# Optimization experiments

Hardware: AMD Instinct MI355X
Metric: run time of the kernel (lower is better)

## Reference

```python
import jax, jax.numpy as jnp
import numpy as np

NP_, NB_, E_, BE_ = 10000, 30000, 300000, 8192
PIN, BIN, EA = 128, 128, 16
HID, GH = 64, 4
D, TH, L, NC, SEQ = 128, 4, 2, 10, 6


def _ln(x, g, b, eps=1e-5):
    m = x.mean(-1, keepdims=True)
    v = ((x - m) ** 2).mean(-1, keepdims=True)
    return (x - m) * jax.lax.rsqrt(v + eps) * g + b


def _seg_softmax(e, seg, n):
    m = jax.ops.segment_max(e, seg, num_segments=n)
    m = jnp.where(jnp.isfinite(m), m, 0.0)
    ex = jnp.exp(e - m[seg])
    s = jax.ops.segment_sum(ex, seg, num_segments=n)
    return ex / (s[seg] + 1e-16)


def _gatv2(xs, xd, es, ed, ea, Wl, bl, Wr, br, We, att, bias, n_dst):
    # PyG GATv2Conv, concat=False, add_self_loops=False, eval mode (no dropout)
    xl = (xs @ Wl + bl).reshape(-1, GH, HID)   # [Ns,H,C] source transform (message content)
    xr = (xd @ Wr + br).reshape(-1, GH, HID)   # [Nd,H,C] dest transform
    eh = (ea @ We).reshape(-1, GH, HID)        # [E,H,C] edge transform (no bias in PyG)
    msg = xl[es] + xr[ed] + eh                 # [E,H,C]
    score = jnp.einsum('ehc,hc->eh', jax.nn.leaky_relu(msg, 0.2), att)
    alpha = _seg_softmax(score, ed, n_dst)     # softmax over in-edges per dest node
    out = jax.ops.segment_sum(alpha[..., None] * xl[es], ed, num_segments=n_dst)
    return out.mean(axis=1) + bias             # concat=False -> mean over heads


def _mha(x, Wqkv, bqkv, Wo, bo):
    S, d = x.shape
    dh = d // TH
    q, k, v = jnp.split(x @ Wqkv + bqkv, 3, axis=-1)
    q = q.reshape(S, TH, dh).transpose(1, 0, 2)
    k = k.reshape(S, TH, dh).transpose(1, 0, 2)
    v = v.reshape(S, TH, dh).transpose(1, 0, 2)
    a = jax.nn.softmax(jnp.einsum('hqd,hkd->hqk', q, k) / jnp.sqrt(jnp.float32(dh)), axis=-1)
    o = jnp.einsum('hqk,hkd->hqd', a, v).transpose(1, 0, 2).reshape(S, d)
    return o @ Wo + bo


def _forward(pitcher_feat, batter_feat, edge_attr, history_states,
             Wp, bp, Wb, bb,
             rel_Wl, rel_bl, rel_Wr, rel_br, rel_We, rel_att, rel_bias,
             rev_Wl, rev_bl, rev_Wr, rev_br, rev_We, rev_att, rev_bias,
             Wgs, bgs, Wet, bet, pos,
             Wqkv, bqkv, Wo, bo, ln1g, ln1b, W1, b1, W2, b2, ln2g, ln2b,
             Wc1, bc1, Wc2, bc2,
             edge_src, edge_dst, edge_ids):
    gelu = lambda t: jax.nn.gelu(t, approximate=False)
    px = gelu(pitcher_feat @ Wp + bp)
    bx = gelu(batter_feat @ Wb + bb)
    # ('pitcher','faces','batter'): messages pitcher->batter, aggregated at batter nodes
    h_b = gelu(_gatv2(px, bx, edge_src, edge_dst, edge_attr,
                      rel_Wl, rel_bl, rel_Wr, rel_br, rel_We, rel_att, rel_bias, bx.shape[0]))
    # reversed relation: batter->pitcher, aggregated at pitcher nodes
    h_p = gelu(_gatv2(bx, px, edge_dst, edge_src, edge_attr,
                      rev_Wl, rev_bl, rev_Wr, rev_br, rev_We, rev_att, rev_bias, px.shape[0]))
    state = jnp.concatenate([h_p.mean(0), h_b.mean(0), edge_attr.mean(0)], -1) @ Wgs + bgs
    tok = jnp.concatenate([h_p[edge_src[edge_ids]], h_b[edge_dst[edge_ids]],
                           edge_attr[edge_ids]], -1) @ Wet + bet
    x = jnp.concatenate([history_states, state[None]], 0) + pos[:SEQ]
    for i in range(L):  # post-LN TransformerEncoderLayer, gelu activation, eval (no dropout)
        x = _ln(x + _mha(x, Wqkv[i], bqkv[i], Wo[i], bo[i]), ln1g[i], ln1b[i])
        f = gelu(x @ W1[i] + b1[i]) @ W2[i] + b2[i]
        x = _ln(x + f, ln2g[i], ln2b[i])
    ctx = x[-1]
    cat = jnp.concatenate([tok, jnp.broadcast_to(ctx, (tok.shape[0], D))], -1)
    return gelu(cat @ Wc1 + bc1) @ Wc2 + bc2


def setup_inputs() -> dict:
    key = jax.random.key(0)
    ks = iter(jax.random.split(key, 64))
    nrm = lambda shape, s: jax.random.normal(next(ks), shape, dtype=jnp.float32) * s
    d = {
        'pitcher_feat': nrm((NP_, PIN), 1.0),
        'batter_feat': nrm((NB_, BIN), 1.0),
        'edge_attr': nrm((E_, EA), 1.0),
        'history_states': nrm((SEQ - 1, D), 1.0),
        'Wp': nrm((PIN, HID), 0.05), 'bp': jnp.zeros((HID,), jnp.float32),
        'Wb': nrm((BIN, HID), 0.05), 'bb': jnp.zeros((HID,), jnp.float32),
    }
    for p in ('rel', 'rev'):
        d[p + '_Wl'] = nrm((HID, GH * HID), 0.05)
        d[p + '_bl'] = jnp.zeros((GH * HID,), jnp.float32)
        d[p + '_Wr'] = nrm((HID, GH * HID), 0.05)
        d[p + '_br'] = jnp.zeros((GH * HID,), jnp.float32)
        d[p + '_We'] = nrm((EA, GH * HID), 0.05)
        d[p + '_att'] = nrm((GH, HID), 0.05)
        d[p + '_bias'] = jnp.zeros((HID,), jnp.float32)
    cin = 2 * HID + EA
    d['Wgs'] = nrm((cin, D), 0.05); d['bgs'] = jnp.zeros((D,), jnp.float32)
    d['Wet'] = nrm((cin, D), 0.05); d['bet'] = jnp.zeros((D,), jnp.float32)
    d['pos'] = nrm((SEQ, D), 0.02)
    d['Wqkv'] = nrm((L, D, 3 * D), 0.05); d['bqkv'] = jnp.zeros((L, 3 * D), jnp.float32)
    d['Wo'] = nrm((L, D, D), 0.05); d['bo'] = jnp.zeros((L, D), jnp.float32)
    d['ln1g'] = jnp.ones((L, D), jnp.float32); d['ln1b'] = jnp.zeros((L, D), jnp.float32)
    d['W1'] = nrm((L, D, 4 * D), 0.05); d['b1'] = jnp.zeros((L, 4 * D), jnp.float32)
    d['W2'] = nrm((L, 4 * D, D), 0.05); d['b2'] = jnp.zeros((L, D), jnp.float32)
    d['ln2g'] = jnp.ones((L, D), jnp.float32); d['ln2b'] = jnp.zeros((L, D), jnp.float32)
    d['Wc1'] = nrm((2 * D, D), 0.05); d['bc1'] = jnp.zeros((D,), jnp.float32)
    d['Wc2'] = nrm((D, NC), 0.05); d['bc2'] = jnp.zeros((NC,), jnp.float32)
    d['edge_src'] = jax.random.randint(next(ks), (E_,), 0, NP_)
    d['edge_dst'] = jax.random.randint(next(ks), (E_,), 0, NB_)
    d['edge_ids'] = jax.random.randint(next(ks), (BE_,), 0, E_)
    return d


def reference(pitcher_feat, batter_feat, edge_attr, history_states,
              Wp, bp, Wb, bb,
              rel_Wl, rel_bl, rel_Wr, rel_br, rel_We, rel_att, rel_bias,
              rev_Wl, rev_bl, rev_Wr, rev_br, rev_We, rev_att, rev_bias,
              Wgs, bgs, Wet, bet, pos,
              Wqkv, bqkv, Wo, bo, ln1g, ln1b, W1, b1, W2, b2, ln2g, ln2b,
              Wc1, bc1, Wc2, bc2,
              edge_src, edge_dst, edge_ids):
    return _forward(pitcher_feat, batter_feat, edge_attr, history_states,
                    Wp, bp, Wb, bb,
                    rel_Wl, rel_bl, rel_Wr, rel_br, rel_We, rel_att, rel_bias,
                    rev_Wl, rev_bl, rev_Wr, rev_br, rev_We, rev_att, rev_bias,
                    Wgs, bgs, Wet, bet, pos,
                    Wqkv, bqkv, Wo, bo, ln1g, ln1b, W1, b1, W2, b2, ln2g, ln2b,
                    Wc1, bc1, Wc2, bc2,
                    edge_src, edge_dst, edge_ids)
```

## Files before the change

### kernel.cpp

```cpp
#include <hip/hip_runtime.h>
#include <math.h>

#define NP 10000
#define NB 30000
#define NEDGE 300000
#define BEDGE 8192
#define EAD 16
#define HID 64
#define GH 4
#define CW 256
#define DD 128
#define SEQ 6
#define NCLS 10
#define L 2
#define NEACOL 64

#if defined(__has_builtin)
#  if __has_builtin(__builtin_amdgcn_fdot2)
#    define HAVE_DOT2 1
#  else
#    define HAVE_DOT2 0
#  endif
#else
#  define HAVE_DOT2 0
// ... 355 lines not shown
    sWeH[i] = __builtin_bit_cast(int,
        __builtin_amdgcn_cvt_pkrtz(We[(2*j)*CW + c], We[(2*j+1)*CW + c]));
  }
#else
  for (int i = t*4; i < 16*CW; i += 1024)
    *(float4*)&sWeH[i] = *(const float4*)&We[i];
#endif
  __syncthreads();
  float4 at = *(const float4*)&att[4*l];
  float4 bi = *(const float4*)&bias[(l & 15)*4];
  float cs0 = 0.f, cs1 = 0.f, cs2 = 0.f, cs3 = 0.f;
  int wid = bid*4 + (t >> 6);
  int nw = nblk*4;
  for (int d = wid; d < ndst; d += nw){
    ushort4 ru = *(const ushort4*)(xr + (size_t)d*CW + 4*l);
    float r0 = b2f(ru.x), r1 = b2f(ru.y), r2 = b2f(ru.z), r3 = b2f(ru.w);
    int rs = row_start[d], re = row_start[d+1];
    float s = 0.f;
    float a0 = 0.f, a1 = 0.f, a2 = 0.f, a3 = 0.f;
    if (rs < re){
      int last = re - 1;
      #define CLMP(x) ((x) > last ? last : (x))
      int2 qA0 = csr[rs],         qA1 = csr[CLMP(rs+1)];
      int2 qB0 = csr[CLMP(rs+2)], qB1 = csr[CLMP(rs+3)];
      int2 nA0 = csr[CLMP(rs+4)], nA1 = csr[CLMP(rs+5)];
      int2 nB0 = csr[CLMP(rs+6)], nB1 = csr[CLMP(rs+7)];
      ushort4 xA0 = *(const ushort4*)(xl + (size_t)qA0.y*CW + 4*l);
      ushort4 xA1 = *(const ushort4*)(xl + (size_t)qA1.y*CW + 4*l);
      evt_t  evA0 = evload(ea, qA0.x, l);
      evt_t  evA1 = evload(ea, qA1.x, l);
      ushort4 xB0 = *(const ushort4*)(xl + (size_t)qB0.y*CW + 4*l);
      ushort4 xB1 = *(const ushort4*)(xl + (size_t)qB1.y*CW + 4*l);
      evt_t  evB0 = evload(ea, qB0.x, l);
      evt_t  evB1 = evload(ea, qB1.x, l);
      for (int i = rs; i < re; i += 4){
        int2 mA0 = csr[CLMP(i+8)],  mA1 = csr[CLMP(i+9)];
        int2 mB0 = csr[CLMP(i+10)], mB1 = csr[CLMP(i+11)];
        GAT_PAIR(xA0, xA1, evA0, evA1, (i+1 < re), true);
        xA0 = *(const ushort4*)(xl + (size_t)nA0.y*CW + 4*l);
        xA1 = *(const ushort4*)(xl + (size_t)nA1.y*CW + 4*l);
        evA0 = evload(ea, nA0.x, l);
        evA1 = evload(ea, nA1.x, l);
        nA0 = mA0; nA1 = mA1;
        GAT_PAIR(xB0, xB1, evB0, evB1, (i+3 < re), (i+2 < re));
        xB0 = *(const ushort4*)(xl + (size_t)nB0.y*CW + 4*l);
        xB1 = *(const ushort4*)(xl + (size_t)nB1.y*CW + 4*l);
        evB0 = evload(ea, nB0.x, l);
        evB1 = evload(ea, nB1.x, l);
        nB0 = mB0; nB1 = mB1;
      }
      #undef CLMP
    }
    float inv = 1.f / (s + 1e-16f);
    float v0 = a0*inv, v1 = a1*inv, v2 = a2*inv, v3 = a3*inv;
    v0 += __shfl_xor(v0, 16); v1 += __shfl_xor(v1, 16);
    v2 += __shfl_xor(v2, 16); v3 += __shfl_xor(v3, 16);
    v0 += __shfl_xor(v0, 32); v1 += __shfl_xor(v1, 32);
    v2 += __shfl_xor(v2, 32); v3 += __shfl_xor(v3, 32);
    if (l < 16){
      float4 o;
      o.x = geluf(v0*0.25f + bi.x);
      o.y = geluf(v1*0.25f + bi.y);
      o.z = geluf(v2*0.25f + bi.z);
      o.w = geluf(v3*0.25f + bi.w);
      *(float4*)(hout + (size_t)d*HID + 4*l) = o;
      cs0 += o.x; cs1 += o.y; cs2 += o.z; cs3 += o.w;
    }
  }
  int w = t >> 6;
  if (l < 16){
    csum[w][l][0] = cs0; csum[w][l][1] = cs1;
    csum[w][l][2] = cs2; csum[w][l][3] = cs3;
  }
  __syncthreads();
  if (t < 64){
    int lq = t >> 2, j = t & 3;
    float sum = csum[0][lq][j] + csum[1][lq][j] + csum[2][lq][j] + csum[3][lq][j];
    float scale = isA ? (1.f/NB) : (1.f/NP);
    float* dst = isA ? (mvec + 64) : mvec;
    atomicAdd(&dst[t], sum * scale);
  }
}

__device__ void gemmcat_body(int bid, const float* __restrict__ hp, const float* __restrict__ hb,
                             const float* __restrict__ ea, const int* __restrict__ esrc,
                             const int* __restrict__ edst, const int* __restrict__ eids,
                             const float* __restrict__ W, const float* __restrict__ bias,
                             float* __restrict__ out)
{
  __shared__ float sAT[16][68];
  __shared__ float sB[16][68];
  __shared__ int sS[64], sD[64], sE[64];
  int t = threadIdx.x;
  int m0 = (bid >> 1)*64, n0 = (bid & 1)*64;
  if (t < 64){
    int e = eids[m0 + t];
    sS[t] = esrc[e]; sD[t] = edst[e]; sE[t] = e;
  }
  __syncthreads();
  int tr = t >> 4, tc = t & 15;
  float acc[4][4] = {};
  for (int k0 = 0; k0 < 144; k0 += 16){
    {
      int r = t >> 2, c = (t & 3) * 4;
      const float* src; int col = k0 + c;
      if (k0 < 64)       { src = hp + (size_t)sS[r]*HID; }
      else if (k0 < 128) { src = hb + (size_t)sD[r]*HID; col -= 64; }
      else               { src = ea + (size_t)sE[r]*EAD; col -= 128; }
      float4 va = *(const float4*)(src + col);
      sAT[c+0][r] = va.x; sAT[c+1][r] = va.y; sAT[c+2][r] = va.z; sAT[c+3][r] = va.w;
    }
    {
      int r = t >> 4, c = (t & 15) * 4;
      float4 vb = *(const float4*)(W + (size_t)(k0+r)*DD + n0 + c);
      *(float4*)&sB[r][c] = vb;
    }
    __syncthreads();
    #pragma unroll
    for (int k = 0; k < 16; ++k){
      float4 av = *(const float4*)&sAT[k][tr*4];
      float4 bv = *(const float4*)&sB[k][tc*4];
      acc[0][0] = fmaf(av.x, bv.x, acc[0][0]);
      acc[0][1] = fmaf(av.x, bv.y, acc[0][1]);
      acc[0][2] = fmaf(av.x, bv.z, acc[0][2]);
      acc[0][3] = fmaf(av.x, bv.w, acc[0][3]);
      acc[1][0] = fmaf(av.y, bv.x, acc[1][0]);
      acc[1][1] = fmaf(av.y, bv.y, acc[1][1]);
      acc[1][2] = fmaf(av.y, bv.z, acc[1][2]);
      acc[1][3] = fmaf(av.y, bv.w, acc[1][3]);
      acc[2][0] = fmaf(av.z, bv.x, acc[2][0]);
      acc[2][1] = fmaf(av.z, bv.y, acc[2][1]);
      acc[2][2] = fmaf(av.z, bv.z, acc[2][2]);
      acc[2][3] = fmaf(av.z, bv.w, acc[2][3]);
      acc[3][0] = fmaf(av.w, bv.x, acc[3][0]);
      acc[3][1] = fmaf(av.w, bv.y, acc[3][1]);
      acc[3][2] = fmaf(av.w, bv.z, acc[3][2]);
      acc[3][3] = fmaf(av.w, bv.w, acc[3][3]);
    }
    __syncthreads();
  }
  #pragma unroll
  for (int i = 0; i < 4; ++i){
    int gr = m0 + tr*4 + i;
    float4 v;
    v.x = acc[i][0] + bias[n0 + tc*4 + 0];
    v.y = acc[i][1] + bias[n0 + tc*4 + 1];
    v.z = acc[i][2] + bias[n0 + tc*4 + 2];
    v.w = acc[i][3] + bias[n0 + tc*4 + 3];
    *(float4*)(out + (size_t)gr*DD + n0 + tc*4) = v;
  }
}

__global__ __launch_bounds__(256)
void gemmcat_kernel(const float* __restrict__ hp, const float* __restrict__ hb,
                    const float* __restrict__ ea, const int* __restrict__ esrc,
                    const int* __restrict__ edst, const int* __restrict__ eids,
                    const float* __restrict__ Wet, const float* __restrict__ bet,
                    float* __restrict__ tokb)
{
  gemmcat_body(blockIdx.x, hp, hb, ea, esrc, edst, eids, Wet, bet, tokb);
}

template<int K, int N, int NC>
__device__ __forceinline__ void qstageF(const float* __restrict__ x,
                                        const float* __restrict__ W,
                                        float (&a)[6][4], int q, int ch)
{
  constexpr int NQ = N/4;
  constexpr int KC = K/NC;
  constexpr int J  = KC/4;
  const float4* wp = (const float4*)W + (size_t)(ch*KC)*NQ + q;
  const float* xb = x + ch*KC;
  float4 wv[KC];
  int kx[J];
  #pragma unroll
  for (int j = 0; j < J; ++j){
    int k4 = (j + ch) & (J-1);
    kx[j] = k4;
    wv[j*4+0] = wp[(size_t)(k4*4+0)*NQ];
    wv[j*4+1] = wp[(size_t)(k4*4+1)*NQ];
    wv[j*4+2] = wp[(size_t)(k4*4+2)*NQ];
    wv[j*4+3] = wp[(size_t)(k4*4+3)*NQ];
  }
  #pragma unroll
  for (int s = 0; s < 6; ++s){ a[s][0]=0.f; a[s][1]=0.f; a[s][2]=0.f; a[s][3]=0.f; }
  #pragma unroll
  for (int j = 0; j < J; ++j){
    #pragma unroll
    for (int s = 0; s < 6; ++s){
      float4 xv = *(const float4*)&xb[s*K + kx[j]*4];
      a[s][0]=fmaf(xv.x,wv[j*4+0].x,a[s][0]); a[s][0]=fmaf(xv.y,wv[j*4+1].x,a[s][0]);
      a[s][0]=fmaf(xv.z,wv[j*4+2].x,a[s][0]); a[s][0]=fmaf(xv.w,wv[j*4+3].x,a[s][0]);
      a[s][1]=fmaf(xv.x,wv[j*4+0].y,a[s][1]); a[s][1]=fmaf(xv.y,wv[j*4+1].y,a[s][1]);
      a[s][1]=fmaf(xv.z,wv[j*4+2].y,a[s][1]); a[s][1]=fmaf(xv.w,wv[j*4+3].y,a[s][1]);
      a[s][2]=fmaf(xv.x,wv[j*4+0].z,a[s][2]); a[s][2]=fmaf(xv.y,wv[j*4+1].z,a[s][2]);
      a[s][2]=fmaf(xv.z,wv[j*4+2].z,a[s][2]); a[s][2]=fmaf(xv.w,wv[j*4+3].z,a[s][2]);
      a[s][3]=fmaf(xv.x,wv[j*4+0].w,a[s][3]); a[s][3]=fmaf(xv.y,wv[j*4+1].w,a[s][3]);
      a[s][3]=fmaf(xv.z,wv[j*4+2].w,a[s][3]); a[s][3]=fmaf(xv.w,wv[j*4+3].w,a[s][3]);
    }
  }
  #pragma unroll
  for (int off = 1; off < NC; off <<= 1){
    #pragma unroll
    for (int s = 0; s < 6; ++s){
      a[s][0]+=__shfl_xor(a[s][0],off); a[s][1]+=__shfl_xor(a[s][1],off);
      a[s][2]+=__shfl_xor(a[s][2],off); a[s][3]+=__shfl_xor(a[s][3],off);
    }
  }
}

__global__ __launch_bounds__(512)
void xform_kernel(const float* __restrict__ hist, const float* __restrict__ mvec,
                  const float* __restrict__ Wgs, const float* __restrict__ bgs,
                  const float* __restrict__ pos,
                  const float* __restrict__ Wqkv, const float* __restrict__ bqkv,
                  const float* __restrict__ Wo, const float* __restrict__ bo,
                  const float* __restrict__ ln1g, const float* __restrict__ ln1b,
                  const float* __restrict__ W1, const float* __restrict__ b1,
                  const float* __restrict__ W2, const float* __restrict__ b2,
                  const float* __restrict__ ln2g, const float* __restrict__ ln2b,
                  const float* __restrict__ Wc1, const float* __restrict__ bc1,
                  float* __restrict__ bias2)
{
  __shared__ float sx[SEQ*DD];
  __shared__ float sq[SEQ*3*DD];
  __shared__ float sh[SEQ*512];
  __shared__ float st[SEQ*DD];
  __shared__ float sc[4][6][6];
  __shared__ float smv[144];
  int t = threadIdx.x;

  for (int i = t; i < (SEQ-1)*DD; i += 512) sx[i] = hist[i] + pos[i];
  if (t < 144) smv[t] = mvec[t];
  __syncthreads();
  if (t < 256){
    int q = t >> 3, ch = t & 7;
    float4 wv[18];
    #pragma unroll
    for (int kk = 0; kk < 18; ++kk)
      wv[kk] = *(const float4*)&Wgs[(ch*18+kk)*DD + q*4];
    float a0=0.f,a1=0.f,a2=0.f,a3=0.f;
    #pragma unroll
    for (int kk = 0; kk < 18; ++kk){
      float xv = smv[ch*18+kk];
      a0=fmaf(xv,wv[kk].x,a0); a1=fmaf(xv,wv[kk].y,a1);
      a2=fmaf(xv,wv[kk].z,a2); a3=fmaf(xv,wv[kk].w,a3);
    }
    #pragma unroll
    for (int off = 1; off < 8; off <<= 1){
      a0+=__shfl_xor(a0,off); a1+=__shfl_xor(a1,off);
      a2+=__shfl_xor(a2,off); a3+=__shfl_xor(a3,off);
    }
    if (ch == 0){
      int n = q*4, base = (SEQ-1)*DD + n;
      sx[base+0]=a0+bgs[n+0]+pos[base+0];
      sx[base+1]=a1+bgs[n+1]+pos[base+1];
      sx[base+2]=a2+bgs[n+2]+pos[base+2];
      sx[base+3]=a3+bgs[n+3]+pos[base+3];
    }
  }
  __syncthreads();

  for (int lyr = 0; lyr < L; ++lyr){
    if (t < 384){
      int q = t >> 2, ch = t & 3;
      const float* wq = Wqkv + (size_t)lyr*DD*3*DD;
      const float* bq = bqkv + lyr*3*DD;
      float a[6][4];
      qstageF<128,384,4>(sx, wq, a, q, ch);
      if (ch == 0){
        int n = q*4;
        #pragma unroll
        for (int s = 0; s < 6; ++s){
          sq[s*384+n+0]=a[s][0]+bq[n+0];
          sq[s*384+n+1]=a[s][1]+bq[n+1];
          sq[s*384+n+2]=a[s][2]+bq[n+2];
          sq[s*384+n+3]=a[s][3]+bq[n+3];
        }
      }
    }
    __syncthreads();
    if (t < 144){
      int h = t/36, r = t%36, qi = r/6, ki = r%6;
      float acc = 0.f;
      #pragma unroll
      for (int d2 = 0; d2 < 32; ++d2)
        acc = fmaf(sq[qi*384 + h*32 + d2], sq[ki*384 + 128 + h*32 + d2], acc);
      sc[h][qi][ki] = acc * 0.17677669529663687f;
    }
    __syncthreads();
    if (t < 24){
      int h = t/6, qi = t%6;
      float* row = sc[h][qi];
      float mx = row[0];
      #pragma unroll
      for (int k = 1; k < 6; ++k) mx = fmaxf(mx, row[k]);
      float sm = 0.f;
      #pragma unroll
      for (int k = 0; k < 6; ++k){ row[k] = __expf(row[k]-mx); sm += row[k]; }
      float inv = 1.f/sm;
      #pragma unroll
      for (int k = 0; k < 6; ++k) row[k] *= inv;
    }
    __syncthreads();
    for (int i = t; i < SEQ*DD; i += 512){
      int s = i >> 7, n = i & 127, h = n >> 5, d2 = n & 31;
      float acc = 0.f;
      #pragma unroll
      for (int ki = 0; ki < 6; ++ki)
        acc = fmaf(sc[h][s][ki], sq[ki*384 + 256 + h*32 + d2], acc);
      st[i] = acc;
    }
    __syncthreads();
    {
      int q = t >> 4, ch = t & 15;
      float a[6][4];
      qstageF<128,128,16>(st, Wo + (size_t)lyr*DD*DD, a, q, ch);
      if (ch == 0){
        int n = q*4;
        const float* bop = bo + lyr*DD;
        #pragma unroll
        for (int s = 0; s < 6; ++s){
          sh[s*128+n+0]=a[s][0]+bop[n+0]+sx[s*128+n+0];
          sh[s*128+n+1]=a[s][1]+bop[n+1]+sx[s*128+n+1];
          sh[s*128+n+2]=a[s][2]+bop[n+2]+sx[s*128+n+2];
          sh[s*128+n+3]=a[s][3]+bop[n+3]+sx[s*128+n+3];
        }
      }
    }
    __syncthreads();
    {
      int w = t >> 6, lw = t & 63;
      if (w < SEQ){
        const float* g = ln1g + lyr*DD; const float* be = ln1b + lyr*DD;
        float v0 = sh[w*DD + lw], v1 = sh[w*DD + 64 + lw];
        float sm = v0 + v1;
        #pragma unroll
        for (int off = 1; off < 64; off <<= 1) sm += __shfl_xor(sm, off);
        float mean = sm * 0.0078125f;
        float d0 = v0-mean, d1 = v1-mean;
        float qv = d0*d0 + d1*d1;
        #pragma unroll
        for (int off = 1; off < 64; off <<= 1) qv += __shfl_xor(qv, off);
        float inv = rsqrtf(qv*0.0078125f + 1e-5f);
        sx[w*DD + lw]      = d0*inv*g[lw] + be[lw];
        sx[w*DD + 64 + lw] = d1*inv*g[64+lw] + be[64+lw];
      }
    }
    __syncthreads();
    {
      int q = t >> 2, ch = t & 3;
      const float* w1 = W1 + (size_t)lyr*DD*512;
      const float* b1p = b1 + lyr*512;
      float a[6][4];
      qstageF<128,512,4>(sx, w1, a, q, ch);
      if (ch == 0){
        int n = q*4;
        #pragma unroll
        for (int s = 0; s < 6; ++s){
          sh[s*512+n+0]=geluf(a[s][0]+b1p[n+0]);
          sh[s*512+n+1]=geluf(a[s][1]+b1p[n+1]);
          sh[s*512+n+2]=geluf(a[s][2]+b1p[n+2]);
          sh[s*512+n+3]=geluf(a[s][3]+b1p[n+3]);
        }
      }
    }
    __syncthreads();
    {
      int q = t >> 4, ch = t & 15;
      const float* w2 = W2 + (size_t)lyr*512*DD;
      const float* b2p = b2 + lyr*DD;
      float a[6][4];
      qstageF<512,128,16>(sh, w2, a, q, ch);
      if (ch == 0){
        int n = q*4;
        #pragma unroll
        for (int s = 0; s < 6; ++s){
          st[s*128+n+0]=a[s][0]+b2p[n+0]+sx[s*128+n+0];
          st[s*128+n+1]=a[s][1]+b2p[n+1]+sx[s*128+n+1];
          st[s*128+n+2]=a[s][2]+b2p[n+2]+sx[s*128+n+2];
          st[s*128+n+3]=a[s][3]+b2p[n+3]+sx[s*128+n+3];
        }
      }
    }
    __syncthreads();
    {
      int w = t >> 6, lw = t & 63;
      if (w < SEQ){
        const float* g = ln2g + lyr*DD; const float* be = ln2b + lyr*DD;
        float v0 = st[w*DD + lw], v1 = st[w*DD + 64 + lw];
        float sm = v0 + v1;
        #pragma unroll
        for (int off = 1; off < 64; off <<= 1) sm += __shfl_xor(sm, off);
        float mean = sm * 0.0078125f;
        float d0 = v0-mean, d1 = v1-mean;
        float qv = d0*d0 + d1*d1;
        #pragma unroll
        for (int off = 1; off < 64; off <<= 1) qv += __shfl_xor(qv, off);
        float inv = rsqrtf(qv*0.0078125f + 1e-5f);
        sx[w*DD + lw]      = d0*inv*g[lw] + be[lw];
        sx[w*DD + 64 + lw] = d1*inv*g[64+lw] + be[64+lw];
      }
    }
    __syncthreads();
  }
  if (t < 256){
    int q = t >> 3, ch = t & 7;
    const float4* wp = (const float4*)(Wc1 + (size_t)DD*DD) + (size_t)(ch*16)*32 + q;
    const float* xb = &sx[(SEQ-1)*DD + ch*16];
    float4 wv[16];
    int kx[4];
    #pragma unroll
    for (int j = 0; j < 4; ++j){
      int k4 = (j + ch) & 3;
      kx[j] = k4;
      wv[j*4+0] = wp[(size_t)(k4*4+0)*32];
      wv[j*4+1] = wp[(size_t)(k4*4+1)*32];
      wv[j*4+2] = wp[(size_t)(k4*4+2)*32];
      wv[j*4+3] = wp[(size_t)(k4*4+3)*32];
    }
    float a0=0.f,a1=0.f,a2=0.f,a3=0.f;
    #pragma unroll
    for (int j = 0; j < 4; ++j){
      float4 xv = *(const float4*)&xb[kx[j]*4];
      a0=fmaf(xv.x,wv[j*4+0].x,a0); a0=fmaf(xv.y,wv[j*4+1].x,a0);
      a0=fmaf(xv.z,wv[j*4+2].x,a0); a0=fmaf(xv.w,wv[j*4+3].x,a0);
      a1=fmaf(xv.x,wv[j*4+0].y,a1); a1=fmaf(xv.y,wv[j*4+1].y,a1);
      a1=fmaf(xv.z,wv[j*4+2].y,a1); a1=fmaf(xv.w,wv[j*4+3].y,a1);
      a2=fmaf(xv.x,wv[j*4+0].z,a2); a2=fmaf(xv.y,wv[j*4+1].z,a2);
      a2=fmaf(xv.z,wv[j*4+2].z,a2); a2=fmaf(xv.w,wv[j*4+3].z,a2);
      a3=fmaf(xv.x,wv[j*4+0].w,a3); a3=fmaf(xv.y,wv[j*4+1].w,a3);
      a3=fmaf(xv.z,wv[j*4+2].w,a3); a3=fmaf(xv.w,wv[j*4+3].w,a3);
    }
    #pragma unroll
    for (int off = 1; off < 8; off <<= 1){
      a0+=__shfl_xor(a0,off); a1+=__shfl_xor(a1,off);
      a2+=__shfl_xor(a2,off); a3+=__shfl_xor(a3,off);
    }
    if (ch == 0){
      int n = q*4;
      bias2[n+0]=a0+bc1[n+0];
      bias2[n+1]=a1+bc1[n+1];
      bias2[n+2]=a2+bc1[n+2];
      bias2[n+3]=a3+bc1[n+3];
    }
  }
}

__global__ __launch_bounds__(256)
void cls_kernel(const float* __restrict__ A, const float* __restrict__ W,
                const float* __restrict__ bias2, const float* __restrict__ Wc2,
                const float* __restrict__ bc2, float* __restrict__ out)
{
  __shared__ float sAT[16][68];
  __shared__ float sB[16][132];
  __shared__ float sH[64][129];
  int t = threadIdx.x;
  int m0 = blockIdx.x * 64;
  int tr = t >> 4, tc = t & 15;
  float acc[4][8] = {};
  for (int k0 = 0; k0 < DD; k0 += 16){
    {
      int r = t >> 2, c = (t & 3) * 4;
      float4 va = *(const float4*)(A + (size_t)(m0+r)*DD + k0 + c);
      sAT[c+0][r] = va.x; sAT[c+1][r] = va.y; sAT[c+2][r] = va.z; sAT[c+3][r] = va.w;
    }
    {
      int r = t >> 4, c = (t & 15) * 8;
      float4 b0 = *(const float4*)(W + (size_t)(k0+r)*DD + c);
      float4 b1 = *(const float4*)(W + (size_t)(k0+r)*DD + c + 4);
      *(float4*)&sB[r][c] = b0;
      *(float4*)&sB[r][c+4] = b1;
    }
    __syncthreads();
    #pragma unroll
    for (int k = 0; k < 16; ++k){
      float4 av = *(const float4*)&sAT[k][tr*4];
      float4 b0 = *(const float4*)&sB[k][tc*8];
      float4 b1 = *(const float4*)&sB[k][tc*8+4];
      #pragma unroll
      for (int i = 0; i < 4; ++i){
        float avi = (i==0)?av.x:(i==1)?av.y:(i==2)?av.z:av.w;
        acc[i][0] = fmaf(avi, b0.x, acc[i][0]);
        acc[i][1] = fmaf(avi, b0.y, acc[i][1]);
        acc[i][2] = fmaf(avi, b0.z, acc[i][2]);
        acc[i][3] = fmaf(avi, b0.w, acc[i][3]);
        acc[i][4] = fmaf(avi, b1.x, acc[i][4]);
        acc[i][5] = fmaf(avi, b1.y, acc[i][5]);
        acc[i][6] = fmaf(avi, b1.z, acc[i][6]);
        acc[i][7] = fmaf(avi, b1.w, acc[i][7]);
      }
    }
    __syncthreads();
  }
  #pragma unroll
  for (int i = 0; i < 4; ++i){
    #pragma unroll
    for (int j = 0; j < 8; ++j){
      sH[tr*4+i][tc*8+j] = geluf(acc[i][j] + bias2[tc*8+j]);
    }
  }
  __syncthreads();
  if (t < 64){
    float a10[NCLS];
    #pragma unroll
    for (int c = 0; c < NCLS; ++c) a10[c] = bc2[c];
    for (int k = 0; k < DD; ++k){
      float hv = sH[t][k];
      #pragma unroll
      for (int c = 0; c < NCLS; ++c)
        a10[c] = fmaf(hv, Wc2[k*NCLS + c], a10[c]);
    }
    #pragma unroll
    for (int c = 0; c < NCLS; ++c)
      out[(size_t)(m0+t)*NCLS + c] = a10[c];
  }
}

extern "C" void kernel_launch(void* const* d_in, const int* in_sizes, int n_in,
                              void* d_out, int out_size, void* d_ws, size_t ws_size,
                              hipStream_t stream){
  (void)in_sizes; (void)n_in; (void)out_size; (void)ws_size;
  const float* pitcher = (const float*)d_in[0];
  const float* batter  = (const float*)d_in[1];
  const float* eattr   = (const float*)d_in[2];
  const float* hist    = (const float*)d_in[3];
  const float* Wp = (const float*)d_in[4];
  const float* bp = (const float*)d_in[5];
  const float* Wb = (const float*)d_in[6];
  const float* bb = (const float*)d_in[7];
  const float* rel_Wl  = (const float*)d_in[8];
  const float* rel_bl  = (const float*)d_in[9];
  const float* rel_Wr  = (const float*)d_in[10];
  const float* rel_br  = (const float*)d_in[11];
  const float* rel_We  = (const float*)d_in[12];
  const float* rel_att = (const float*)d_in[13];
  const float* rel_bias= (const float*)d_in[14];
  const float* rev_Wl  = (const float*)d_in[15];
  const float* rev_bl  = (const float*)d_in[16];
  const float* rev_Wr  = (const float*)d_in[17];
  const float* rev_br  = (const float*)d_in[18];
  const float* rev_We  = (const float*)d_in[19];
  const float* rev_att = (const float*)d_in[20];
  const float* rev_bias= (const float*)d_in[21];
  const float* Wgs = (const float*)d_in[22];
  const float* bgs = (const float*)d_in[23];
  const float* Wet = (const float*)d_in[24];
  const float* bet = (const float*)d_in[25];
  const float* pos = (const float*)d_in[26];
  const float* Wqkv= (const float*)d_in[27];
  const float* bqkv= (const float*)d_in[28];
  const float* Wo  = (const float*)d_in[29];
  const float* bo  = (const float*)d_in[30];
  const float* ln1g= (const float*)d_in[31];
  const float* ln1b= (const float*)d_in[32];
  const float* W1  = (const float*)d_in[33];
  const float* b1  = (const float*)d_in[34];
  const float* W2  = (const float*)d_in[35];
  const float* b2  = (const float*)d_in[36];
  const float* ln2g= (const float*)d_in[37];
  const float* ln2b= (const float*)d_in[38];
  const float* Wc1 = (const float*)d_in[39];
  const float* bc1 = (const float*)d_in[40];
  const float* Wc2 = (const float*)d_in[41];
  const float* bc2 = (const float*)d_in[42];
  const int* esrc = (const int*)d_in[43];
  const int* edst = (const int*)d_in[44];
  const int* eids = (const int*)d_in[45];

  char* w = (char*)d_ws;
  size_t off = 0;
  auto alloc = [&](size_t bytes)->void*{
    void* p = (void*)(w + off);
    off += (bytes + 255) & ~(size_t)255;
    return p;
  };
  unsigned short* px_bf  = (unsigned short*)alloc((size_t)NP*HID*2);
  unsigned short* bx_bf  = (unsigned short*)alloc((size_t)NB*HID*2);
  float*          hp     = (float*)alloc((size_t)NP*HID*4);
  float*          hb     = (float*)alloc((size_t)NB*HID*4);
  unsigned short* xlA    = (unsigned short*)alloc((size_t)NP*CW*2);
  unsigned short* xrA    = (unsigned short*)alloc((size_t)NB*CW*2);
  unsigned short* xlB    = (unsigned short*)alloc((size_t)NB*CW*2);
  unsigned short* xrB    = (unsigned short*)alloc((size_t)NP*CW*2);
  int*            degAB  = (int*)alloc((size_t)(NB+NP)*4);
  int*            degA   = degAB;
  int*            degB   = degAB + NB;
  int*            rowstA = (int*)alloc((size_t)(NB+1)*4);
  int*            rowstB = (int*)alloc((size_t)(NP+1)*4);
  int*            cursA  = (int*)alloc((size_t)NB*4);
  int*            cursB  = (int*)alloc((size_t)NP*4);
  int2*           csrA   = (int2*)alloc((size_t)NEDGE*8);
  int2*           csrB   = (int2*)alloc((size_t)NEDGE*8);
  float*          mvec   = (float*)alloc(144*4);
  float*          bias2  = (float*)alloc(DD*4);
  float*          tokb   = (float*)xlA;

  const int nbCount = (NEDGE + 255)/256;
  const int nbP = (NP + 63)/64;
  const int nbB = (NB + 63)/64;

  hipMemsetAsync(degAB, 0, (size_t)(NB+NP)*4, stream);
  k1_count_enc<<<nbCount + nbP + nbB, 256, 0, stream>>>(
      edst, esrc, degA, degB,
      pitcher, Wp, bp, px_bf, batter, Wb, bb, bx_bf, nbCount, nbP);

  scan2_kernel<<<2, 1024, 0, stream>>>(degA, rowstA, cursA, NB,
                                       degB, rowstB, cursB, NP, mvec);

  k2_scatter_proj<<<nbCount + 2*nbP + 2*nbB, 256, 0, stream>>>(
      edst, esrc, cursA, cursB, csrA, csrB, px_bf, bx_bf,
      rel_Wl, rel_bl, rel_Wr, rel_br, rev_Wl, rev_bl, rev_Wr, rev_br,
      xlA, xrA, xlB, xrB, nbCount, nbP, nbB);

  gat2_kernel<<<NEACOL + 4096, 256, 0, stream>>>(
      xlA, xrA, rel_We, rel_att, rel_bias, csrA, rowstA, hb,
      xlB, xrB, rev_We, rev_att, rev_bias, csrB, rowstB, hp,
      eattr, mvec, 2048);

  gemmcat_kernel<<<256, 256, 0, stream>>>(
      hp, hb, eattr, esrc, edst, eids, Wet, bet, tokb);

  xform_kernel<<<1, 512, 0, stream>>>(
      hist, mvec, Wgs, bgs, pos, Wqkv, bqkv, Wo, bo, ln1g, ln1b,
      W1, b1, W2, b2, ln2g, ln2b, Wc1, bc1, bias2);

  cls_kernel<<<BEDGE/64, 256, 0, stream>>>(tokb, Wc1, bias2, Wc2, bc2, (float*)d_out);
}
```

Measured before the change: 389.0 us.

## Split single-block transformer kernel into multi-block per-stage kernels

```diff
diff --git a/kernel.cpp b/kernel.cpp
--- a/kernel.cpp
+++ b/kernel.cpp
@@ -531,299 +531,165 @@
 }
 
 __global__ __launch_bounds__(256)
-void gemmcat_kernel(const float* __restrict__ hp, const float* __restrict__ hb,
-                    const float* __restrict__ ea, const int* __restrict__ esrc,
-                    const int* __restrict__ edst, const int* __restrict__ eids,
-                    const float* __restrict__ Wet, const float* __restrict__ bet,
-                    float* __restrict__ tokb)
+void k4_buildx_gemmcat(const float* __restrict__ hist, const float* __restrict__ mvec,
+                       const float* __restrict__ Wgs, const float* __restrict__ bgs,
+                       const float* __restrict__ pos, float* __restrict__ xbuf,
+                       const float* __restrict__ hp, const float* __restrict__ hb,
+                       const float* __restrict__ ea, const int* __restrict__ esrc,
+                       const int* __restrict__ edst, const int* __restrict__ eids,
+                       const float* __restrict__ Wet, const float* __restrict__ bet,
+                       float* __restrict__ tokb)
 {
-  gemmcat_body(blockIdx.x, hp, hb, ea, esrc, edst, eids, Wet, bet, tokb);
-}
-
-template<int K, int N, int NC>
-__device__ __forceinline__ void qstageF(const float* __restrict__ x,
-                                        const float* __restrict__ W,
-                                        float (&a)[6][4], int q, int ch)
-{
-  constexpr int NQ = N/4;
-  constexpr int KC = K/NC;
-  constexpr int J  = KC/4;
-  const float4* wp = (const float4*)W + (size_t)(ch*KC)*NQ + q;
-  const float* xb = x + ch*KC;
-  float4 wv[KC];
-  int kx[J];
+  int t = threadIdx.x;
+  if (blockIdx.x == 0){
+    __shared__ float smv[144];
+    __shared__ float spart[DD];
+    if (t < 144) smv[t] = mvec[t];
+    for (int i = t; i < (SEQ-1)*DD; i += 256) xbuf[i] = hist[i] + pos[i];
+    __syncthreads();
+    int c = t & 127, h = t >> 7;
+    float acc = 0.f;
+    for (int k = h*72; k < h*72 + 72; ++k)
+      acc = fmaf(smv[k], Wgs[(size_t)k*DD + c], acc);
+    if (h == 1) spart[c] = acc;
+    __syncthreads();
+    if (h == 0){
+      int base = (SEQ-1)*DD + c;
+      xbuf[base] = acc + spart[c] + bgs[c] + pos[base];
+    }
+  } else {
+    gemmcat_body(blockIdx.x - 1, hp, hb, ea, esrc, edst, eids, Wet, bet, tokb);
+  }
+}
+
+template<bool GELU>
+__global__ __launch_bounds__(64)
+void lin6_kernel(const float* __restrict__ in, const float* __restrict__ W,
+                 const float* __restrict__ bias, float* __restrict__ out,
+                 int K, int N){
+  __shared__ float sx[SEQ*512];
+  int t = threadIdx.x;
+  for (int i = t; i < SEQ*K; i += 64) sx[i] = in[i];
+  __syncthreads();
+  int n = blockIdx.x*64 + t;
+  float acc[SEQ] = {};
+  for (int k = 0; k < K; ++k){
+    float wv = W[(size_t)k*N + n];
+    #pragma unroll
+    for (int m = 0; m < SEQ; ++m) acc[m] = fmaf(sx[m*K + k], wv, acc[m]);
+  }
+  float bv = bias[n];
   #pragma unroll
-  for (int j = 0; j < J; ++j){
-    int k4 = (j + ch) & (J-1);
-    kx[j] = k4;
-    wv[j*4+0] = wp[(size_t)(k4*4+0)*NQ];
-    wv[j*4+1] = wp[(size_t)(k4*4+1)*NQ];
-    wv[j*4+2] = wp[(size_t)(k4*4+2)*NQ];
-    wv[j*4+3] = wp[(size_t)(k4*4+3)*NQ];
+  for (int m = 0; m < SEQ; ++m){
+    float v = acc[m] + bv;
+    out[m*N + n] = GELU ? geluf(v) : v;
+  }
+}
+
+__global__ __launch_bounds__(256)
+void att6_kernel(const float* __restrict__ qkv, float* __restrict__ so){
+  __shared__ float sq[SEQ*384];
+  __shared__ float sc[4][6][6];
+  int t = threadIdx.x;
+  for (int i = t; i < SEQ*384; i += 256) sq[i] = qkv[i];
+  __syncthreads();
+  if (t < 144){
+    int h = t/36, r = t%36, qi = r/6, ki = r%6;
+    float acc = 0.f;
+    #pragma unroll
+    for (int d = 0; d < 32; ++d)
+      acc = fmaf(sq[qi*384 + h*32 + d], sq[ki*384 + 128 + h*32 + d], acc);
+    sc[h][qi][ki] = acc * 0.17677669529663687f;
+  }
+  __syncthreads();
+  if (t < 24){
+    int h = t/6, qi = t%6;
+    float* row = sc[h][qi];
+    float mx = row[0];
+    #pragma unroll
+    for (int k = 1; k < 6; ++k) mx = fmaxf(mx, row[k]);
+    float sm = 0.f;
+    #pragma unroll
+    for (int k = 0; k < 6; ++k){ row[k] = __expf(row[k]-mx); sm += row[k]; }
+    float inv = 1.f / sm;
+    #pragma unroll
+    for (int k = 0; k < 6; ++k) row[k] *= inv;
+  }
+  __syncthreads();
+  for (int i = t; i < SEQ*DD; i += 256){
+    int s = i / DD, n = i % DD, h = n >> 5, d = n & 31;
+    float acc = 0.f;
+    #pragma unroll
+    for (int ki = 0; ki < 6; ++ki)
+      acc = fmaf(sc[h][s][ki], sq[ki*384 + 256 + h*32 + d], acc);
+    so[i] = acc;
+  }
+}
+
+template<int KS>
+__global__ __launch_bounds__(128)
+void proj_splitk_kernel(const float* __restrict__ A, const float* __restrict__ W,
+                        float* __restrict__ partial){
+  __shared__ float sa[SEQ*KS];
+  int kb = blockIdx.x, t = threadIdx.x;
+  int K = KS * gridDim.x;
+  for (int i = t; i < SEQ*KS; i += 128){
+    int m = i / KS, k = i - m*KS;
+    sa[i] = A[(size_t)m*K + kb*KS + k];
+  }
+  __syncthreads();
+  float acc[SEQ] = {};
+  for (int k = 0; k < KS; ++k){
+    float wv = W[(size_t)(kb*KS + k)*DD + t];
+    #pragma unroll
+    for (int m = 0; m < SEQ; ++m) acc[m] = fmaf(sa[m*KS + k], wv, acc[m]);
   }
   #pragma unroll
-  for (int s = 0; s < 6; ++s){ a[s][0]=0.f; a[s][1]=0.f; a[s][2]=0.f; a[s][3]=0.f; }
+  for (int m = 0; m < SEQ; ++m)
+    partial[(size_t)kb*SEQ*DD + m*DD + t] = acc[m];
+}
+
+__global__ __launch_bounds__(128)
+void resln_kernel(const float* __restrict__ partial, int nkb,
+                  const float* __restrict__ b, const float* __restrict__ resid,
+                  const float* __restrict__ g, const float* __restrict__ be,
+                  float* __restrict__ out){
+  __shared__ float sr[SEQ][DD];
+  __shared__ float smean[SEQ], sinv[SEQ];
+  int t = threadIdx.x;
+  float bv = b[t];
   #pragma unroll
-  for (int j = 0; j < J; ++j){
-    #pragma unroll
-    for (int s = 0; s < 6; ++s){
-      float4 xv = *(const float4*)&xb[s*K + kx[j]*4];
-      a[s][0]=fmaf(xv.x,wv[j*4+0].x,a[s][0]); a[s][0]=fmaf(xv.y,wv[j*4+1].x,a[s][0]);
-      a[s][0]=fmaf(xv.z,wv[j*4+2].x,a[s][0]); a[s][0]=fmaf(xv.w,wv[j*4+3].x,a[s][0]);
-      a[s][1]=fmaf(xv.x,wv[j*4+0].y,a[s][1]); a[s][1]=fmaf(xv.y,wv[j*4+1].y,a[s][1]);
-      a[s][1]=fmaf(xv.z,wv[j*4+2].y,a[s][1]); a[s][1]=fmaf(xv.w,wv[j*4+3].y,a[s][1]);
-      a[s][2]=fmaf(xv.x,wv[j*4+0].z,a[s][2]); a[s][2]=fmaf(xv.y,wv[j*4+1].z,a[s][2]);
-      a[s][2]=fmaf(xv.z,wv[j*4+2].z,a[s][2]); a[s][2]=fmaf(xv.w,wv[j*4+3].z,a[s][2]);
-      a[s][3]=fmaf(xv.x,wv[j*4+0].w,a[s][3]); a[s][3]=fmaf(xv.y,wv[j*4+1].w,a[s][3]);
-      a[s][3]=fmaf(xv.z,wv[j*4+2].w,a[s][3]); a[s][3]=fmaf(xv.w,wv[j*4+3].w,a[s][3]);
-    }
-  }
+  for (int m = 0; m < SEQ; ++m){
+    float acc = resid[m*DD + t] + bv;
+    for (int kb = 0; kb < nkb; ++kb) acc += partial[(size_t)kb*SEQ*DD + m*DD + t];
+    sr[m][t] = acc;
+  }
+  __syncthreads();
+  if (t < SEQ){
+    const float* r = sr[t];
+    float mean = 0.f;
+    for (int k = 0; k < DD; ++k) mean += r[k];
+    mean *= (1.f/DD);
+    float var = 0.f;
+    for (int k = 0; k < DD; ++k){ float dv = r[k]-mean; var += dv*dv; }
+    smean[t] = mean;
+    sinv[t]  = rsqrtf(var*(1.f/DD) + 1e-5f);
+  }
+  __syncthreads();
+  float gv = g[t], bev = be[t];
   #pragma unroll
-  for (int off = 1; off < NC; off <<= 1){
-    #pragma unroll
-    for (int s = 0; s < 6; ++s){
-      a[s][0]+=__shfl_xor(a[s][0],off); a[s][1]+=__shfl_xor(a[s][1],off);
-      a[s][2]+=__shfl_xor(a[s][2],off); a[s][3]+=__shfl_xor(a[s][3],off);
-    }
-  }
-}
-
-__global__ __launch_bounds__(512)
-void xform_kernel(const float* __restrict__ hist, const float* __restrict__ mvec,
-                  const float* __restrict__ Wgs, const float* __restrict__ bgs,
-                  const float* __restrict__ pos,
-                  const float* __restrict__ Wqkv, const float* __restrict__ bqkv,
-                  const float* __restrict__ Wo, const float* __restrict__ bo,
-                  const float* __restrict__ ln1g, const float* __restrict__ ln1b,
-                  const float* __restrict__ W1, const float* __restrict__ b1,
-                  const float* __restrict__ W2, const float* __restrict__ b2,
-                  const float* __restrict__ ln2g, const float* __restrict__ ln2b,
-                  const float* __restrict__ Wc1, const float* __restrict__ bc1,
-                  float* __restrict__ bias2)
-{
-  __shared__ float sx[SEQ*DD];
-  __shared__ float sq[SEQ*3*DD];
-  __shared__ float sh[SEQ*512];
-  __shared__ float st[SEQ*DD];
-  __shared__ float sc[4][6][6];
-  __shared__ float smv[144];
-  int t = threadIdx.x;
-
-  for (int i = t; i < (SEQ-1)*DD; i += 512) sx[i] = hist[i] + pos[i];
-  if (t < 144) smv[t] = mvec[t];
-  __syncthreads();
-  if (t < 256){
-    int q = t >> 3, ch = t & 7;
-    float4 wv[18];
-    #pragma unroll
-    for (int kk = 0; kk < 18; ++kk)
-      wv[kk] = *(const float4*)&Wgs[(ch*18+kk)*DD + q*4];
-    float a0=0.f,a1=0.f,a2=0.f,a3=0.f;
-    #pragma unroll
-    for (int kk = 0; kk < 18; ++kk){
-      float xv = smv[ch*18+kk];
-      a0=fmaf(xv,wv[kk].x,a0); a1=fmaf(xv,wv[kk].y,a1);
-      a2=fmaf(xv,wv[kk].z,a2); a3=fmaf(xv,wv[kk].w,a3);
-    }
-    #pragma unroll
-    for (int off = 1; off < 8; off <<= 1){
-      a0+=__shfl_xor(a0,off); a1+=__shfl_xor(a1,off);
-      a2+=__shfl_xor(a2,off); a3+=__shfl_xor(a3,off);
-    }
-    if (ch == 0){
-      int n = q*4, base = (SEQ-1)*DD + n;
-      sx[base+0]=a0+bgs[n+0]+pos[base+0];
-      sx[base+1]=a1+bgs[n+1]+pos[base+1];
-      sx[base+2]=a2+bgs[n+2]+pos[base+2];
-      sx[base+3]=a3+bgs[n+3]+pos[base+3];
-    }
-  }
-  __syncthreads();
-
-  for (int lyr = 0; lyr < L; ++lyr){
-    if (t < 384){
-      int q = t >> 2, ch = t & 3;
-      const float* wq = Wqkv + (size_t)lyr*DD*3*DD;
-      const float* bq = bqkv + lyr*3*DD;
-      float a[6][4];
-      qstageF<128,384,4>(sx, wq, a, q, ch);
-      if (ch == 0){
-        int n = q*4;
-        #pragma unroll
-        for (int s = 0; s < 6; ++s){
-          sq[s*384+n+0]=a[s][0]+bq[n+0];
-          sq[s*384+n+1]=a[s][1]+bq[n+1];
-          sq[s*384+n+2]=a[s][2]+bq[n+2];
-          sq[s*384+n+3]=a[s][3]+bq[n+3];
-        }
-      }
-    }
-    __syncthreads();
-    if (t < 144){
-      int h = t/36, r = t%36, qi = r/6, ki = r%6;
-      float acc = 0.f;
-      #pragma unroll
-      for (int d2 = 0; d2 < 32; ++d2)
-        acc = fmaf(sq[qi*384 + h*32 + d2], sq[ki*384 + 128 + h*32 + d2], acc);
-      sc[h][qi][ki] = acc * 0.17677669529663687f;
-    }
-    __syncthreads();
-    if (t < 24){
-      int h = t/6, qi = t%6;
-      float* row = sc[h][qi];
-      float mx = row[0];
-      #pragma unroll
-      for (int k = 1; k < 6; ++k) mx = fmaxf(mx, row[k]);
-      float sm = 0.f;
-      #pragma unroll
-      for (int k = 0; k < 6; ++k){ row[k] = __expf(row[k]-mx); sm += row[k]; }
-      float inv = 1.f/sm;
-      #pragma unroll
-      for (int k = 0; k < 6; ++k) row[k] *= inv;
-    }
-    __syncthreads();
-    for (int i = t; i < SEQ*DD; i += 512){
-      int s = i >> 7, n = i & 127, h = n >> 5, d2 = n & 31;
-      float acc = 0.f;
-      #pragma unroll
-      for (int ki = 0; ki < 6; ++ki)
-        acc = fmaf(sc[h][s][ki], sq[ki*384 + 256 + h*32 + d2], acc);
-      st[i] = acc;
-    }
-    __syncthreads();
-    {
-      int q = t >> 4, ch = t & 15;
-      float a[6][4];
-      qstageF<128,128,16>(st, Wo + (size_t)lyr*DD*DD, a, q, ch);
-      if (ch == 0){
-        int n = q*4;
-        const float* bop = bo + lyr*DD;
-        #pragma unroll
-        for (int s = 0; s < 6; ++s){
-          sh[s*128+n+0]=a[s][0]+bop[n+0]+sx[s*128+n+0];
-          sh[s*128+n+1]=a[s][1]+bop[n+1]+sx[s*128+n+1];
-          sh[s*128+n+2]=a[s][2]+bop[n+2]+sx[s*128+n+2];
-          sh[s*128+n+3]=a[s][3]+bop[n+3]+sx[s*128+n+3];
-        }
-      }
-    }
-    __syncthreads();
-    {
-      int w = t >> 6, lw = t & 63;
-      if (w < SEQ){
-        const float* g = ln1g + lyr*DD; const float* be = ln1b + lyr*DD;
-        float v0 = sh[w*DD + lw], v1 = sh[w*DD + 64 + lw];
-        float sm = v0 + v1;
-        #pragma unroll
-        for (int off = 1; off < 64; off <<= 1) sm += __shfl_xor(sm, off);
-        float mean = sm * 0.0078125f;
-        float d0 = v0-mean, d1 = v1-mean;
-        float qv = d0*d0 + d1*d1;
-        #pragma unroll
-        for (int off = 1; off < 64; off <<= 1) qv += __shfl_xor(qv, off);
-        float inv = rsqrtf(qv*0.0078125f + 1e-5f);
-        sx[w*DD + lw]      = d0*inv*g[lw] + be[lw];
-        sx[w*DD + 64 + lw] = d1*inv*g[64+lw] + be[64+lw];
-      }
-    }
-    __syncthreads();
-    {
-      int q = t >> 2, ch = t & 3;
-      const float* w1 = W1 + (size_t)lyr*DD*512;
-      const float* b1p = b1 + lyr*512;
-      float a[6][4];
-      qstageF<128,512,4>(sx, w1, a, q, ch);
-      if (ch == 0){
-        int n = q*4;
-        #pragma unroll
-        for (int s = 0; s < 6; ++s){
-          sh[s*512+n+0]=geluf(a[s][0]+b1p[n+0]);
-          sh[s*512+n+1]=geluf(a[s][1]+b1p[n+1]);
-          sh[s*512+n+2]=geluf(a[s][2]+b1p[n+2]);
-          sh[s*512+n+3]=geluf(a[s][3]+b1p[n+3]);
-        }
-      }
-    }
-    __syncthreads();
-    {
-      int q = t >> 4, ch = t & 15;
-      const float* w2 = W2 + (size_t)lyr*512*DD;
-      const float* b2p = b2 + lyr*DD;
-      float a[6][4];
-      qstageF<512,128,16>(sh, w2, a, q, ch);
-      if (ch == 0){
-        int n = q*4;
-        #pragma unroll
-        for (int s = 0; s < 6; ++s){
-          st[s*128+n+0]=a[s][0]+b2p[n+0]+sx[s*128+n+0];
-          st[s*128+n+1]=a[s][1]+b2p[n+1]+sx[s*128+n+1];
-          st[s*128+n+2]=a[s][2]+b2p[n+2]+sx[s*128+n+2];
-          st[s*128+n+3]=a[s][3]+b2p[n+3]+sx[s*128+n+3];
-        }
-      }
-    }
-    __syncthreads();
-    {
-      int w = t >> 6, lw = t & 63;
-      if (w < SEQ){
-        const float* g = ln2g + lyr*DD; const float* be = ln2b + lyr*DD;
-        float v0 = st[w*DD + lw], v1 = st[w*DD + 64 + lw];
-        float sm = v0 + v1;
-        #pragma unroll
-        for (int off = 1; off < 64; off <<= 1) sm += __shfl_xor(sm, off);
-        float mean = sm * 0.0078125f;
-        float d0 = v0-mean, d1 = v1-mean;
-        float qv = d0*d0 + d1*d1;
-        #pragma unroll
-        for (int off = 1; off < 64; off <<= 1) qv += __shfl_xor(qv, off);
-        float inv = rsqrtf(qv*0.0078125f + 1e-5f);
-        sx[w*DD + lw]      = d0*inv*g[lw] + be[lw];
-        sx[w*DD + 64 + lw] = d1*inv*g[64+lw] + be[64+lw];
-      }
-    }
-    __syncthreads();
-  }
-  if (t < 256){
-    int q = t >> 3, ch = t & 7;
-    const float4* wp = (const float4*)(Wc1 + (size_t)DD*DD) + (size_t)(ch*16)*32 + q;
-    const float* xb = &sx[(SEQ-1)*DD + ch*16];
-    float4 wv[16];
-    int kx[4];
-    #pragma unroll
-    for (int j = 0; j < 4; ++j){
-      int k4 = (j + ch) & 3;
-      kx[j] = k4;
-      wv[j*4+0] = wp[(size_t)(k4*4+0)*32];
-      wv[j*4+1] = wp[(size_t)(k4*4+1)*32];
-      wv[j*4+2] = wp[(size_t)(k4*4+2)*32];
-      wv[j*4+3] = wp[(size_t)(k4*4+3)*32];
-    }
-    float a0=0.f,a1=0.f,a2=0.f,a3=0.f;
-    #pragma unroll
-    for (int j = 0; j < 4; ++j){
-      float4 xv = *(const float4*)&xb[kx[j]*4];
-      a0=fmaf(xv.x,wv[j*4+0].x,a0); a0=fmaf(xv.y,wv[j*4+1].x,a0);
-      a0=fmaf(xv.z,wv[j*4+2].x,a0); a0=fmaf(xv.w,wv[j*4+3].x,a0);
-      a1=fmaf(xv.x,wv[j*4+0].y,a1); a1=fmaf(xv.y,wv[j*4+1].y,a1);
-      a1=fmaf(xv.z,wv[j*4+2].y,a1); a1=fmaf(xv.w,wv[j*4+3].y,a1);
-      a2=fmaf(xv.x,wv[j*4+0].z,a2); a2=fmaf(xv.y,wv[j*4+1].z,a2);
-      a2=fmaf(xv.z,wv[j*4+2].z,a2); a2=fmaf(xv.w,wv[j*4+3].z,a2);
-      a3=fmaf(xv.x,wv[j*4+0].w,a3); a3=fmaf(xv.y,wv[j*4+1].w,a3);
-      a3=fmaf(xv.z,wv[j*4+2].w,a3); a3=fmaf(xv.w,wv[j*4+3].w,a3);
-    }
-    #pragma unroll
-    for (int off = 1; off < 8; off <<= 1){
-      a0+=__shfl_xor(a0,off); a1+=__shfl_xor(a1,off);
-      a2+=__shfl_xor(a2,off); a3+=__shfl_xor(a3,off);
-    }
-    if (ch == 0){
-      int n = q*4;
-      bias2[n+0]=a0+bc1[n+0];
-      bias2[n+1]=a1+bc1[n+1];
-      bias2[n+2]=a2+bc1[n+2];
-      bias2[n+3]=a3+bc1[n+3];
-    }
-  }
+  for (int m = 0; m < SEQ; ++m)
+    out[m*DD + t] = (sr[m][t]-smean[m])*sinv[m]*gv + bev;
+}
+
+__global__ __launch_bounds__(64)
+void ctxdot_kernel(const float* __restrict__ ctx, const float* __restrict__ Wc1,
+                   const float* __restrict__ bc1, float* __restrict__ bias2){
+  int n = blockIdx.x*64 + threadIdx.x;
+  float acc = bc1[n];
+  for (int k = 0; k < DD; ++k)
+    acc = fmaf(ctx[k], Wc1[(size_t)(DD + k)*DD + n], acc);
+  bias2[n] = acc;
 }
 
 __global__ __launch_bounds__(256)
@@ -973,6 +839,11 @@
   int2*           csrB   = (int2*)alloc((size_t)NEDGE*8);
   float*          mvec   = (float*)alloc(144*4);
   float*          bias2  = (float*)alloc(DD*4);
+  float*          xbuf   = (float*)alloc(SEQ*DD*4);
+  float*          qkvb   = (float*)alloc(SEQ*3*DD*4);
+  float*          sob    = (float*)alloc(SEQ*DD*4);
+  float*          ffnb   = (float*)alloc(SEQ*4*DD*4);
+  float*          partial= (float*)alloc(8*SEQ*DD*4);
   float*          tokb   = (float*)xlA;
 
   const int nbCount = (NEDGE + 255)/256;
@@ -997,12 +868,25 @@
       xlB, xrB, rev_We, rev_att, rev_bias, csrB, rowstB, hp,
       eattr, mvec, 2048);
 
-  gemmcat_kernel<<<256, 256, 0, stream>>>(
+  k4_buildx_gemmcat<<<257, 256, 0, stream>>>(
+      hist, mvec, Wgs, bgs, pos, xbuf,
       hp, hb, eattr, esrc, edst, eids, Wet, bet, tokb);
 
-  xform_kernel<<<1, 512, 0, stream>>>(
-      hist, mvec, Wgs, bgs, pos, Wqkv, bqkv, Wo, bo, ln1g, ln1b,
-      W1, b1, W2, b2, ln2g, ln2b, Wc1, bc1, bias2);
-
+  for (int l = 0; l < L; ++l){
+    lin6_kernel<false><<<6, 64, 0, stream>>>(xbuf, Wqkv + (size_t)l*DD*3*DD,
+                                             bqkv + (size_t)l*3*DD, qkvb, DD, 3*DD);
+    att6_kernel<<<1, 256, 0, stream>>>(qkvb, sob);
+    proj_splitk_kernel<32><<<4, 128, 0, stream>>>(sob, Wo + (size_t)l*DD*DD, partial);
+    resln_kernel<<<1, 128, 0, stream>>>(partial, 4, bo + (size_t)l*DD, xbuf,
+                                        ln1g + (size_t)l*DD, ln1b + (size_t)l*DD, xbuf);
+    lin6_kernel<true><<<8, 64, 0, stream>>>(xbuf, W1 + (size_t)l*DD*512,
+                                            b1 + (size_t)l*512, ffnb, DD, 512);
+    proj_splitk_kernel<64><<<8, 128, 0, stream>>>(ffnb, W2 + (size_t)l*512*DD, partial);
+    resln_kernel<<<1, 128, 0, stream>>>(partial, 8, b2 + (size_t)l*DD, xbuf,
+                                        ln2g + (size_t)l*DD, ln2b + (size_t)l*DD, xbuf);
+  }
+  const float* ctxb = xbuf + 5*DD;
+
+  ctxdot_kernel<<<2, 64, 0, stream>>>(ctxb, Wc1, bc1, bias2);
   cls_kernel<<<BEDGE/64, 256, 0, stream>>>(tokb, Wc1, bias2, Wc2, bc2, (float*)d_out);
 }
```

Result: slower. 437.3 us (+12.4%).
